# Kernel optimization log

Hardware: AMD Instinct MI355X
Metric: run time of the kernel (lower is better)

The kernel has to match this reference:

```python
import jax, jax.numpy as jnp
import numpy as np

N = 4            # polynomial points per segment
SEGMENTS = 32
LENGTH = 2.0
HALF = 0.5 * LENGTH
IN_CH = 32
OUT_CH = 32
BATCH = 16
NODES = 1024


def _cheb_points(n):
    # Chebyshev-Lobatto points on [-1, 1] (LagrangePoly basis nodes)
    return -np.cos(np.pi * np.arange(n) / (n - 1))


def setup_inputs() -> dict:
    key = jax.random.key(0)
    k1, k2 = jax.random.split(key)
    x = jax.random.normal(k1, (BATCH, IN_CH, NODES), dtype=jnp.float32)
    # w.data.uniform_(-weight_magnitude, weight_magnitude)
    w = jax.random.uniform(k2, (OUT_CH, IN_CH, (N - 1) * SEGMENTS + 1),
                           dtype=jnp.float32, minval=-1.0, maxval=1.0)
    return {"x": x, "w": w}


def _lagrange_basis(x_in):
    # x_in: [b, c, m] -> basis values [b, c, m, n]
    X = jnp.asarray(_cheb_points(N), dtype=x_in.dtype)
    cols = []
    for j in range(N):
        b = jnp.ones_like(x_in)
        for m in range(N):
            if m != j:
                b = b * (x_in - X[m]) / (X[j] - X[m])
        cols.append(b)
    return jnp.stack(cols, axis=-1)


def reference(x, w):
    # bin index per element, clamped to valid segments
    id_min = jnp.clip(((x + HALF) / LENGTH * SEGMENTS).astype(jnp.int32), 0, SEGMENTS - 1)
    id_max = id_min + 1
    wid_min = id_min * (N - 1)                         # [b, c, m]
    idx = wid_min[..., None] + jnp.arange(N)           # [b, c, m, n]
    c_idx = jnp.arange(IN_CH)[None, :, None, None]     # broadcast channel index
    wg = w[:, c_idx, idx]                              # [o, b, c, m, n] irregular gather
    wg = jnp.transpose(wg, (1, 0, 2, 3, 4))            # [b, o, c, m, n]
    # map x into the local segment coordinate in [-half, half]
    x_min = id_min.astype(x.dtype) / SEGMENTS * 2.0 - 1.0
    x_max = id_max.astype(x.dtype) / SEGMENTS * 2.0 - 1.0
    x_in = LENGTH * (x - x_min) / (x_max - x_min) - HALF
    basis = _lagrange_basis(x_in)                      # [b, c, m, n]
    # sum over in_channels and polynomial points -> [b, o, m]
    return jnp.einsum('bcmj,bocmj->bom', basis, wg)
```

## Files before the change

kernel.cpp:

```cpp
#include <hip/hip_runtime.h>

#define NB 16
#define NC 32
#define NO 32
#define NM 1024
#define SEGS 32
#define WLEN 97

__global__ __launch_bounds__(256) void repack_w_kernel(const float* __restrict__ w,
                                                       float4* __restrict__ w3) {
    int i = blockIdx.x * blockDim.x + threadIdx.x;
    if (i >= NC * SEGS * NO) return;
    int o   = i & 31;
    int seg = (i >> 5) & 31;
    int c   = i >> 10;
    const float* p = w + (o * NC + c) * WLEN + 3 * seg;
    w3[i] = make_float4(p[0], p[1], p[2], p[3]);
}

template <bool USE_W3>
__global__ __launch_bounds__(256) void pw_main_kernel(const float* __restrict__ x,
                                                      const float* __restrict__ w,
                                                      const float4* __restrict__ w3,
                                                      float* __restrict__ out) {
    const int blk = blockIdx.x;
    const int b   = blk >> 7;
    const int m0  = (blk & 127) * 8;

    __shared__ float4 sb[NC][8];
    __shared__ int    sseg[NC][8];

    const int tid = threadIdx.x;

    {
        const int c  = tid >> 3;
        const int mt = tid & 7;
        const float xv = x[(b * NC + c) * NM + m0 + mt];

        float v  = (xv + 1.0f) * 16.0f;
        int   id = (int)v;
        id = min(max(id, 0), SEGS - 1);

        const float x_min = (float)id * 0.0625f - 1.0f;
        const float t     = (xv - x_min) * 32.0f - 1.0f;

        const float d0 = t + 1.0f;
        const float d1 = t + 0.5f;
        const float d2 = t - 0.5f;
        const float d3 = t - 1.0f;
        float4 bb;
        bb.x = d1 * d2 * d3 * (-0.66666667f);
        bb.y = d0 * d2 * d3 * ( 1.33333333f);
        bb.z = d0 * d1 * d3 * (-1.33333333f);
        bb.w = d0 * d1 * d2 * ( 0.66666667f);

        sb[c][mt]   = bb;
        sseg[c][mt] = id;
    }
    __syncthreads();

    const int o  = tid & 31;
    const int mt = tid >> 5;

    float acc = 0.0f;
#pragma unroll
    for (int c = 0; c < NC; ++c) {
        const float4 bb = sb[c][mt];
        const int    sg = sseg[c][mt];
        float4 wv;
        if (USE_W3) {
            wv = w3[(c * SEGS + sg) * NO + o];
        } else {
            const float* p = w + (o * NC + c) * WLEN + 3 * sg;
            wv = make_float4(p[0], p[1], p[2], p[3]);
        }
        acc = fmaf(bb.x, wv.x, acc);
        acc = fmaf(bb.y, wv.y, acc);
        acc = fmaf(bb.z, wv.z, acc);
        acc = fmaf(bb.w, wv.w, acc);
    }

    out[(b * NO + o) * NM + m0 + mt] = acc;
}

extern "C" void kernel_launch(void* const* d_in, const int* in_sizes, int n_in,
                              void* d_out, int out_size, void* d_ws, size_t ws_size,
                              hipStream_t stream) {
    const float* x = (const float*)d_in[0];
    const float* w = (const float*)d_in[1];
    float* out = (float*)d_out;

    const size_t w3_bytes = (size_t)NC * SEGS * NO * sizeof(float4);

    if (ws_size >= w3_bytes) {
        float4* w3 = (float4*)d_ws;
        repack_w_kernel<<<(NC * SEGS * NO + 255) / 256, 256, 0, stream>>>(w, w3);
        pw_main_kernel<true><<<NB * (NM / 8), 256, 0, stream>>>(x, w, w3, out);
    } else {
        pw_main_kernel<false><<<NB * (NM / 8), 256, 0, stream>>>(x, w, nullptr, out);
    }
}
```

Before: 67.89 us.

## Widen per-block tile to 16 points with two outputs per thread and precomputed offsets

The main kernel now covers 16 node positions per block and gives each thread two output channels (op and op+16), so every basis value read from shared memory is reused for two weight loads. Gather offsets for each point are precomputed in shared memory and loaded as int4 vectors into registers, which takes the index arithmetic out of the inner loop. Each block does twice the work, so the grid has half as many blocks. The cost is higher register use and fewer blocks in flight, and the fallback path becomes a separate simpler kernel.

```diff
diff --git a/kernel.cpp b/kernel.cpp
--- a/kernel.cpp
+++ b/kernel.cpp
@@ -6,6 +6,7 @@
 #define NM 1024
 #define SEGS 32
 #define WLEN 97
+#define MT 16
 
 __global__ __launch_bounds__(256) void repack_w_kernel(const float* __restrict__ w,
                                                        float4* __restrict__ w3) {
@@ -18,69 +19,112 @@
     w3[i] = make_float4(p[0], p[1], p[2], p[3]);
 }
 
-template <bool USE_W3>
+__device__ __forceinline__ float4 lagrange_basis(float xv, int& id_out) {
+    float v  = (xv + 1.0f) * 16.0f;
+    int   id = (int)v;
+    id = min(max(id, 0), SEGS - 1);
+    const float x_min = (float)id * 0.0625f - 1.0f;
+    const float t     = (xv - x_min) * 32.0f - 1.0f;
+    const float d0 = t + 1.0f;
+    const float d1 = t + 0.5f;
+    const float d2 = t - 0.5f;
+    const float d3 = t - 1.0f;
+    float4 bb;
+    bb.x = d1 * d2 * d3 * (-0.66666667f);
+    bb.y = d0 * d2 * d3 * ( 1.33333333f);
+    bb.z = d0 * d1 * d3 * (-1.33333333f);
+    bb.w = d0 * d1 * d2 * ( 0.66666667f);
+    id_out = id;
+    return bb;
+}
+
 __global__ __launch_bounds__(256) void pw_main_kernel(const float* __restrict__ x,
-                                                      const float* __restrict__ w,
                                                       const float4* __restrict__ w3,
                                                       float* __restrict__ out) {
     const int blk = blockIdx.x;
-    const int b   = blk >> 7;
-    const int m0  = (blk & 127) * 8;
+    const int b   = blk >> 6;
+    const int m0  = (blk & 63) * MT;
 
-    __shared__ float4 sb[NC][8];
-    __shared__ int    sseg[NC][8];
+    __shared__ float4 sb[NC][17];
+    __shared__ int    soff[MT][36];
 
     const int tid = threadIdx.x;
 
     {
-        const int c  = tid >> 3;
-        const int mt = tid & 7;
-        const float xv = x[(b * NC + c) * NM + m0 + mt];
-
-        float v  = (xv + 1.0f) * 16.0f;
-        int   id = (int)v;
-        id = min(max(id, 0), SEGS - 1);
-
-        const float x_min = (float)id * 0.0625f - 1.0f;
-        const float t     = (xv - x_min) * 32.0f - 1.0f;
-
-        const float d0 = t + 1.0f;
-        const float d1 = t + 0.5f;
-        const float d2 = t - 0.5f;
-        const float d3 = t - 1.0f;
-        float4 bb;
-        bb.x = d1 * d2 * d3 * (-0.66666667f);
-        bb.y = d0 * d2 * d3 * ( 1.33333333f);
-        bb.z = d0 * d1 * d3 * (-1.33333333f);
-        bb.w = d0 * d1 * d2 * ( 0.66666667f);
-
-        sb[c][mt]   = bb;
-        sseg[c][mt] = id;
+        const int c   = tid >> 3;
+        const int mtb = tid & 7;
+#pragma unroll
+        for (int k = 0; k < 2; ++k) {
+            const int mt = mtb + 8 * k;
+            const float xv = x[(b * NC + c) * NM + m0 + mt];
+            int id;
+            float4 bb = lagrange_basis(xv, id);
+            sb[c][mt]   = bb;
+            soff[mt][c] = (c * SEGS + id) * NO;
+        }
     }
     __syncthreads();
 
-    const int o  = tid & 31;
-    const int mt = tid >> 5;
+    const int lane = tid & 63;
+    const int wid  = tid >> 6;
+    const int op   = lane & 15;
+    const int mt   = wid * 4 + (lane >> 4);
+
+    int4 offs[8];
+    {
+        const int4* sp = (const int4*)&soff[mt][0];
+#pragma unroll
+        for (int k = 0; k < 8; ++k) offs[k] = sp[k];
+    }
+
+    const float4* __restrict__ wp = w3 + op;
+
+    float acc0 = 0.0f, acc1 = 0.0f;
+#pragma unroll
+    for (int k = 0; k < 8; ++k) {
+        const int4 o4 = offs[k];
+#pragma unroll
+        for (int j = 0; j < 4; ++j) {
+            const int c    = 4 * k + j;
+            const int base = (j == 0) ? o4.x : (j == 1) ? o4.y : (j == 2) ? o4.z : o4.w;
+            const float4 bb  = sb[c][mt];
+            const float4 wv0 = wp[base];
+            const float4 wv1 = wp[base + 16];
+            acc0 = fmaf(bb.x, wv0.x, acc0);
+            acc0 = fmaf(bb.y, wv0.y, acc0);
+            acc0 = fmaf(bb.z, wv0.z, acc0);
+            acc0 = fmaf(bb.w, wv0.w, acc0);
+            acc1 = fmaf(bb.x, wv1.x, acc1);
+            acc1 = fmaf(bb.y, wv1.y, acc1);
+            acc1 = fmaf(bb.z, wv1.z, acc1);
+            acc1 = fmaf(bb.w, wv1.w, acc1);
+        }
+    }
+
+    out[(b * NO + op) * NM + m0 + mt]        = acc0;
+    out[(b * NO + op + 16) * NM + m0 + mt]   = acc1;
+}
+
+__global__ __launch_bounds__(256) void pw_fallback_kernel(const float* __restrict__ x,
+                                                          const float* __restrict__ w,
+                                                          float* __restrict__ out) {
+    const int blk = blockIdx.x;
+    const int b   = blk >> 7;
+    const int m   = (blk & 127) * 8 + (threadIdx.x & 7);
+    const int o   = threadIdx.x >> 3;
 
     float acc = 0.0f;
-#pragma unroll
     for (int c = 0; c < NC; ++c) {
-        const float4 bb = sb[c][mt];
-        const int    sg = sseg[c][mt];
-        float4 wv;
-        if (USE_W3) {
-            wv = w3[(c * SEGS + sg) * NO + o];
-        } else {
-            const float* p = w + (o * NC + c) * WLEN + 3 * sg;
-            wv = make_float4(p[0], p[1], p[2], p[3]);
-        }
-        acc = fmaf(bb.x, wv.x, acc);
-        acc = fmaf(bb.y, wv.y, acc);
-        acc = fmaf(bb.z, wv.z, acc);
-        acc = fmaf(bb.w, wv.w, acc);
+        const float xv = x[(b * NC + c) * NM + m];
+        int id;
+        float4 bb = lagrange_basis(xv, id);
+        const float* p = w + (o * NC + c) * WLEN + 3 * id;
+        acc = fmaf(bb.x, p[0], acc);
+        acc = fmaf(bb.y, p[1], acc);
+        acc = fmaf(bb.z, p[2], acc);
+        acc = fmaf(bb.w, p[3], acc);
     }
-
-    out[(b * NO + o) * NM + m0 + mt] = acc;
+    out[(b * NO + o) * NM + m] = acc;
 }
 
 extern "C" void kernel_launch(void* const* d_in, const int* in_sizes, int n_in,
@@ -95,8 +139,8 @@
     if (ws_size >= w3_bytes) {
         float4* w3 = (float4*)d_ws;
         repack_w_kernel<<<(NC * SEGS * NO + 255) / 256, 256, 0, stream>>>(w, w3);
-        pw_main_kernel<true><<<NB * (NM / 8), 256, 0, stream>>>(x, w, w3, out);
+        pw_main_kernel<<<NB * (NM / MT), 256, 0, stream>>>(x, w3, out);
     } else {
-        pw_main_kernel<false><<<NB * (NM / 8), 256, 0, stream>>>(x, w, nullptr, out);
+        pw_fallback_kernel<<<NB * (NM / 8), 256, 0, stream>>>(x, w, out);
     }
 }
```

Result: no change. 66.57 us (-1.9%).
